# Optimization experiments

Measured on AMD Instinct MI355X. Metric: run time of the kernel, lower is better.

## Reference

```python
import jax, jax.numpy as jnp
import numpy as np


def _div_tree_level(n_agents, level):
    # Deterministic reproduction of get_division_tree (seeded shuffle), row `level`.
    rng = np.random.RandomState(0)
    perm = rng.permutation(n_agents)
    max_div = int(np.ceil(np.log2(n_agents)))
    levels = np.zeros((max_div + 1, n_agents), dtype=np.int64)
    for ith in range(1, max_div + 1):
        levels[ith] = levels[ith - 1]
        for j in range(n_agents):
            seg = j // (n_agents / 2 ** ith)
            if int(seg) % 2 == 1:
                levels[ith, j] += 2 ** (ith - 1)
    res = levels[:, perm]  # res_levels[:, i] = levels[:, agent2divitreeindex[i]]
    return res[level]


def setup_inputs() -> dict:
    B, A, D, H, NA = 4096, 32, 512, 512, 32
    LEVEL = 3  # current_level after change_div_tree_level(3): 8 distinct experts
    key = jax.random.key(0)
    ks = jax.random.split(key, 4)
    x0 = jax.random.normal(ks[0], (B, A, D), dtype=jnp.float32)
    W_shared = jax.random.normal(ks[1], (D, H), dtype=jnp.float32) * 0.02
    b_shared = jnp.zeros((H,), jnp.float32)
    W1 = jax.random.normal(ks[2], (A, H, H), dtype=jnp.float32) * 0.02
    b1 = jnp.zeros((A, H), jnp.float32)
    W2 = jax.random.normal(ks[3], (A, H, NA), dtype=jnp.float32) * 0.02
    b2 = jnp.zeros((A, NA), jnp.float32)
    route = jnp.asarray(_div_tree_level(A, LEVEL), dtype=jnp.int32)  # [A] expert id per agent
    return dict(x0=x0, W_shared=W_shared, b_shared=b_shared,
                W1=W1, b1=b1, W2=W2, b2=b2, route=route)


def reference(x0, W_shared, b_shared, W1, b1, W2, b2, route):
    # shared trunk: Linear + ReLU over all agents at once
    x1 = jax.nn.relu(x0 @ W_shared + b_shared)          # [B, A, H]
    # static MoE dispatch: gather each agent's expert weights, batched GEMM per agent slot
    Wg1, bg1 = W1[route], b1[route]                     # [A, H, H], [A, H]
    Wg2, bg2 = W2[route], b2[route]                     # [A, H, NA], [A, NA]
    h = jax.nn.relu(jnp.einsum('bah,ahk->bak', x1, Wg1) + bg1)   # [B, A, H]
    x2 = jnp.einsum('bah,ahk->bak', h, Wg2) + bg2       # [B, A, NA]
    return x2
```

## Files before the change

### kernel.cpp

```cpp
#include <hip/hip_runtime.h>
#include <cstdint>
#include <cstddef>

typedef __bf16 bf16x8 __attribute__((ext_vector_type(8)));
typedef float f32x4 __attribute__((ext_vector_type(4)));
typedef unsigned short u16;
typedef u16 u16x4 __attribute__((ext_vector_type(4)));
typedef u16 u16x8 __attribute__((ext_vector_type(8)));

__device__ __forceinline__ u16 f2bf(float f) {
  union { float f; unsigned u; } v; v.f = f;
  return (u16)((v.u + 0x7FFFu + ((v.u >> 16) & 1u)) >> 16);
}

__global__ void frag_cvt(const float* __restrict__ in, const int* __restrict__ route,
                         u16* __restrict__ out, int K, int N) {
  const int a = blockIdx.z;
  const int src = route ? route[a] : a;
  const int f = threadIdx.x >> 6, l = threadIdx.x & 63;
  const int r = l & 15, q = l >> 4;
  const int kt = blockIdx.x * 4 + f;
  const int nb = blockIdx.y;
  const int KT = K >> 5, NB = N >> 4;
  const float* ip = in + (size_t)src * K * N + (size_t)(kt * 32 + q * 8) * N + nb * 16 + r;
  u16x8 d;
#pragma unroll
  for (int e = 0; e < 8; ++e) d[e] = f2bf(ip[(size_t)e * N]);
  *(u16x8*)&out[((((size_t)a * NB + nb) * KT + kt) * 64 + l) * 8] = d;
}

__device__ __forceinline__ void gemm64(const u16* __restrict__ Bw, const u16* __restrict__ Xs,
                                       int r, int q, f32x4 acc[4][4]) {
  bf16x8 bcur[4], bnxt[4];
#pragma unroll
  for (int nt = 0; nt < 4; ++nt) bcur[nt] = *(const bf16x8*)(Bw + nt * 8192);
#pragma unroll
  for (int kt = 0; kt < 16; ++kt) {
    if (kt < 15) {
#pragma unroll
      for (int nt = 0; nt < 4; ++nt)
        bnxt[nt] = *(const bf16x8*)(Bw + nt * 8192 + (kt + 1) * 512);
    }
#pragma unroll
    for (int mt = 0; mt < 4; ++mt) {
      const int m = mt * 16 + r;
      const bf16x8 af = *(const bf16x8*)&Xs[m * 512 + ((((kt << 2) + q) ^ (m & 7)) << 3)];
#pragma unroll
      for (int nt = 0; nt < 4; ++nt)
        acc[mt][nt] = __builtin_amdgcn_mfma_f32_16x16x32_bf16(bcur[nt], af, acc[mt][nt], 0, 0, 0);
    }
#pragma unroll
    for (int nt = 0; nt < 4; ++nt) bcur[nt] = bnxt[nt];
  }
}

__device__ __forceinline__ void epi_relu(u16* __restrict__ Xs, const float* __restrict__ bias,
                                         f32x4 acc[4][4], int w, int r, int q) {
#pragma unroll
  for (int mt = 0; mt < 4; ++mt) {
    const int m = mt * 16 + r;
#pragma unroll
    for (int nt = 0; nt < 4; ++nt) {
      const int col = w * 64 + nt * 16 + q * 4;
      const int gp = (col >> 3) ^ (m & 7);
      const float4 bb = *(const float4*)&bias[col];
      const f32x4 v = acc[mt][nt];
      const u16x4 d = { f2bf(fmaxf(v.x + bb.x, 0.f)), f2bf(fmaxf(v.y + bb.y, 0.f)),
                        f2bf(fmaxf(v.z + bb.z, 0.f)), f2bf(fmaxf(v.w + bb.w, 0.f)) };
      *(u16x4*)&Xs[m * 512 + gp * 8 + (q & 1) * 4] = d;
    }
  }
}

__global__ __launch_bounds__(512, 4)
void fused_mlp(const float* __restrict__ X0, const u16* __restrict__ Wsf,
               const float* __restrict__ bsh, const u16* __restrict__ W1f,
               const float* __restrict__ b1, const u16* __restrict__ W2f,
               const float* __restrict__ b2, const int* __restrict__ route,
               float* __restrict__ Out) {
  __shared__ u16 Xs[64 * 512];

  const int tid = threadIdx.x;
  const int w = tid >> 6, l = tid & 63;
  const int r = l & 15, q = l >> 4;

  const int bid = blockIdx.x;
  const int xcd = bid & 7, idx = bid >> 3;
  const int a = (xcd << 2) | (idx >> 6);
  const int b0 = (idx & 63) << 6;
  const int rt = route[a];

  {
    const float* gx = X0 + ((size_t)b0 * 32 + a) * 512;
#pragma unroll
    for (int i = 0; i < 8; ++i) {
      const int lin = i * 512 + tid;
      const int m = lin >> 6, g = lin & 63;
      const float* p = gx + (size_t)m * (32 * 512) + g * 8;
      const float4 u = *(const float4*)p;
      const float4 v = *(const float4*)(p + 4);
      const u16x8 d = { f2bf(u.x), f2bf(u.y), f2bf(u.z), f2bf(u.w),
                        f2bf(v.x), f2bf(v.y), f2bf(v.z), f2bf(v.w) };
      *(u16x8*)&Xs[m * 512 + ((g ^ (m & 7)) << 3)] = d;
    }
  }
  __syncthreads();

  f32x4 acc[4][4];

#pragma unroll
  for (int mt = 0; mt < 4; ++mt)
#pragma unroll
    for (int nt = 0; nt < 4; ++nt) acc[mt][nt] = (f32x4){0.f, 0.f, 0.f, 0.f};
  gemm64(Wsf + (w << 15) + l * 8, Xs, r, q, acc);
  __syncthreads();
  epi_relu(Xs, bsh, acc, w, r, q);
  __syncthreads();

#pragma unroll
  for (int mt = 0; mt < 4; ++mt)
#pragma unroll
    for (int nt = 0; nt < 4; ++nt) acc[mt][nt] = (f32x4){0.f, 0.f, 0.f, 0.f};
  gemm64(W1f + (size_t)a * 262144 + (w << 15) + l * 8, Xs, r, q, acc);
  __syncthreads();
  epi_relu(Xs, b1 + (size_t)rt * 512, acc, w, r, q);
  __syncthreads();

  {
    const int mt3 = w & 3, nt3 = w >> 2;
    const int m = mt3 * 16 + r;
    const u16* B2 = W2f + (size_t)a * 16384 + (nt3 << 13) + l * 8;
    f32x4 o = (f32x4){0.f, 0.f, 0.f, 0.f};
#pragma unroll
    for (int kt = 0; kt < 16; ++kt) {
      const bf16x8 af = *(const bf16x8*)&Xs[m * 512 + ((((kt << 2) + q) ^ (m & 7)) << 3)];
      const bf16x8 bf = *(const bf16x8*)(B2 + (kt << 9));
      o = __builtin_amdgcn_mfma_f32_16x16x32_bf16(bf, af, o, 0, 0, 0);
    }
    const int col = (nt3 << 4) + (q << 2);
    const float4 bb = *(const float4*)&b2[rt * 32 + col];
    const float4 res = { o.x + bb.x, o.y + bb.y, o.z + bb.z, o.w + bb.w };
    *(float4*)&Out[(size_t)(b0 + m) * 1024 + a * 32 + col] = res;
  }
}

extern "C" void kernel_launch(void* const* d_in, const int* in_sizes, int n_in,
                              void* d_out, int out_size, void* d_ws, size_t ws_size,
                              hipStream_t stream) {
  (void)in_sizes; (void)n_in; (void)out_size; (void)ws_size;
  const float* x0  = (const float*)d_in[0];
  const float* Wsh = (const float*)d_in[1];
  const float* bsh = (const float*)d_in[2];
  const float* W1  = (const float*)d_in[3];
  const float* b1  = (const float*)d_in[4];
  const float* W2  = (const float*)d_in[5];
  const float* b2  = (const float*)d_in[6];
  const int* route = (const int*)d_in[7];
  float* out = (float*)d_out;

  char* ws = (char*)d_ws;
  u16* Wsf = (u16*)(ws + 0);
  u16* W1f = (u16*)(ws + 524288);
  u16* W2f = (u16*)(ws + 524288 + 16777216);

  frag_cvt<<<dim3(4, 32, 1),  256, 0, stream>>>(Wsh, nullptr, Wsf, 512, 512);
  frag_cvt<<<dim3(4, 32, 32), 256, 0, stream>>>(W1, route, W1f, 512, 512);
  frag_cvt<<<dim3(4, 2, 32),  256, 0, stream>>>(W2, route, W2f, 512, 32);
  fused_mlp<<<dim3(2048), 512, 0, stream>>>(x0, Wsf, bsh, W1f, b1, W2f, b2, route, out);
}
```

Measured before the change: 555.0 us.

## Double batch tile per block, fragment-major LDS layout, convert only routed experts

The fused MLP kernel now uses 1024-thread blocks covering 128 batch rows per agent, split into 2 M-warpgroups by 8 N-warps. Each weight fragment loaded from global memory is therefore reused across twice as many rows. Activations in LDS are stored in MFMA-fragment-major order instead of a swizzled row layout, so A-fragment loads become contiguous. The weight conversion now converts each distinct expert once, indexed by expert id, and skips experts no agent uses, which cuts redundant conversion traffic. In exchange, the block uses 128KB of LDS and 1024 threads, so occupancy is lower and the grid has fewer blocks.

```diff
diff --git a/kernel.cpp b/kernel.cpp
--- a/kernel.cpp
+++ b/kernel.cpp
@@ -13,24 +13,29 @@
   return (u16)((v.u + 0x7FFFu + ((v.u >> 16) & 1u)) >> 16);
 }
 
-__global__ void frag_cvt(const float* __restrict__ in, const int* __restrict__ route,
+__global__ void frag_cvt(const float* __restrict__ in, const int* __restrict__ sel,
                          u16* __restrict__ out, int K, int N) {
-  const int a = blockIdx.z;
-  const int src = route ? route[a] : a;
+  const int s = blockIdx.z;
+  if (sel) {
+    bool need = false;
+#pragma unroll
+    for (int i = 0; i < 32; ++i) need |= (sel[i] == s);
+    if (!need) return;
+  }
   const int f = threadIdx.x >> 6, l = threadIdx.x & 63;
   const int r = l & 15, q = l >> 4;
   const int kt = blockIdx.x * 4 + f;
   const int nb = blockIdx.y;
   const int KT = K >> 5, NB = N >> 4;
-  const float* ip = in + (size_t)src * K * N + (size_t)(kt * 32 + q * 8) * N + nb * 16 + r;
+  const float* ip = in + (size_t)s * K * N + (size_t)(kt * 32 + q * 8) * N + nb * 16 + r;
   u16x8 d;
 #pragma unroll
   for (int e = 0; e < 8; ++e) d[e] = f2bf(ip[(size_t)e * N]);
-  *(u16x8*)&out[((((size_t)a * NB + nb) * KT + kt) * 64 + l) * 8] = d;
+  *(u16x8*)&out[((((size_t)s * NB + nb) * KT + kt) * 64 + l) * 8] = d;
 }
 
-__device__ __forceinline__ void gemm64(const u16* __restrict__ Bw, const u16* __restrict__ Xs,
-                                       int r, int q, f32x4 acc[4][4]) {
+__device__ __forceinline__ void gemm64(const u16* __restrict__ Bw, const u16* __restrict__ Af,
+                                       f32x4 acc[4][4]) {
   bf16x8 bcur[4], bnxt[4];
 #pragma unroll
   for (int nt = 0; nt < 4; ++nt) bcur[nt] = *(const bf16x8*)(Bw + nt * 8192);
@@ -43,8 +48,7 @@
     }
 #pragma unroll
     for (int mt = 0; mt < 4; ++mt) {
-      const int m = mt * 16 + r;
-      const bf16x8 af = *(const bf16x8*)&Xs[m * 512 + ((((kt << 2) + q) ^ (m & 7)) << 3)];
+      const bf16x8 af = *(const bf16x8*)(Af + kt * 4096 + mt * 512);
 #pragma unroll
       for (int nt = 0; nt < 4; ++nt)
         acc[mt][nt] = __builtin_amdgcn_mfma_f32_16x16x32_bf16(bcur[nt], af, acc[mt][nt], 0, 0, 0);
@@ -55,92 +59,95 @@
 }
 
 __device__ __forceinline__ void epi_relu(u16* __restrict__ Xs, const float* __restrict__ bias,
-                                         f32x4 acc[4][4], int w, int r, int q) {
+                                         f32x4 acc[4][4], int wm, int wn, int r, int q) {
 #pragma unroll
   for (int mt = 0; mt < 4; ++mt) {
-    const int m = mt * 16 + r;
+    const int MT = wm * 4 + mt;
 #pragma unroll
     for (int nt = 0; nt < 4; ++nt) {
-      const int col = w * 64 + nt * 16 + q * 4;
-      const int gp = (col >> 3) ^ (m & 7);
+      const int col = wn * 64 + nt * 16 + q * 4;
+      const int kt2 = col >> 5;
+      const int q2 = (col >> 3) & 3;
       const float4 bb = *(const float4*)&bias[col];
       const f32x4 v = acc[mt][nt];
       const u16x4 d = { f2bf(fmaxf(v.x + bb.x, 0.f)), f2bf(fmaxf(v.y + bb.y, 0.f)),
                         f2bf(fmaxf(v.z + bb.z, 0.f)), f2bf(fmaxf(v.w + bb.w, 0.f)) };
-      *(u16x4*)&Xs[m * 512 + gp * 8 + (q & 1) * 4] = d;
+      *(u16x4*)&Xs[((kt2 * 8 + MT) * 64 + q2 * 16 + r) * 8 + (q & 1) * 4] = d;
     }
   }
 }
 
-__global__ __launch_bounds__(512, 4)
+__global__ __launch_bounds__(1024, 4)
 void fused_mlp(const float* __restrict__ X0, const u16* __restrict__ Wsf,
                const float* __restrict__ bsh, const u16* __restrict__ W1f,
                const float* __restrict__ b1, const u16* __restrict__ W2f,
                const float* __restrict__ b2, const int* __restrict__ route,
                float* __restrict__ Out) {
-  __shared__ u16 Xs[64 * 512];
+  __shared__ u16 Xs[65536];
 
   const int tid = threadIdx.x;
   const int w = tid >> 6, l = tid & 63;
   const int r = l & 15, q = l >> 4;
+  const int wm = w >> 3, wn = w & 7;
 
   const int bid = blockIdx.x;
   const int xcd = bid & 7, idx = bid >> 3;
-  const int a = (xcd << 2) | (idx >> 6);
-  const int b0 = (idx & 63) << 6;
+  const int a = (xcd << 2) | (idx >> 5);
+  const int b0 = (idx & 31) << 7;
   const int rt = route[a];
 
   {
-    const float* gx = X0 + ((size_t)b0 * 32 + a) * 512;
+    const int m = ((w & 7) << 4) + r;
+    const float* p = X0 + ((size_t)b0 * 32 + a) * 512 + (size_t)m * 16384
+                   + ((w >> 3) << 8) + (q << 3);
+    const int ktb = (w >> 3) << 3;
 #pragma unroll
     for (int i = 0; i < 8; ++i) {
-      const int lin = i * 512 + tid;
-      const int m = lin >> 6, g = lin & 63;
-      const float* p = gx + (size_t)m * (32 * 512) + g * 8;
-      const float4 u = *(const float4*)p;
-      const float4 v = *(const float4*)(p + 4);
+      const float4 u = *(const float4*)(p + i * 32);
+      const float4 v = *(const float4*)(p + i * 32 + 4);
       const u16x8 d = { f2bf(u.x), f2bf(u.y), f2bf(u.z), f2bf(u.w),
                         f2bf(v.x), f2bf(v.y), f2bf(v.z), f2bf(v.w) };
-      *(u16x8*)&Xs[m * 512 + ((g ^ (m & 7)) << 3)] = d;
+      *(u16x8*)&Xs[((ktb + i) * 8 + (w & 7)) * 512 + l * 8] = d;
     }
   }
   __syncthreads();
 
   f32x4 acc[4][4];
+  const u16* Af = Xs + (wm << 11) + l * 8;
 
 #pragma unroll
   for (int mt = 0; mt < 4; ++mt)
 #pragma unroll
     for (int nt = 0; nt < 4; ++nt) acc[mt][nt] = (f32x4){0.f, 0.f, 0.f, 0.f};
-  gemm64(Wsf + (w << 15) + l * 8, Xs, r, q, acc);
+  gemm64(Wsf + (wn << 15) + l * 8, Af, acc);
   __syncthreads();
-  epi_relu(Xs, bsh, acc, w, r, q);
+  epi_relu(Xs, bsh, acc, wm, wn, r, q);
   __syncthreads();
 
 #pragma unroll
   for (int mt = 0; mt < 4; ++mt)
 #pragma unroll
     for (int nt = 0; nt < 4; ++nt) acc[mt][nt] = (f32x4){0.f, 0.f, 0.f, 0.f};
-  gemm64(W1f + (size_t)a * 262144 + (w << 15) + l * 8, Xs, r, q, acc);
+  gemm64(W1f + ((size_t)rt << 18) + (wn << 15) + l * 8, Af, acc);
   __syncthreads();
-  epi_relu(Xs, b1 + (size_t)rt * 512, acc, w, r, q);
+  epi_relu(Xs, b1 + (size_t)rt * 512, acc, wm, wn, r, q);
   __syncthreads();
 
   {
-    const int mt3 = w & 3, nt3 = w >> 2;
-    const int m = mt3 * 16 + r;
-    const u16* B2 = W2f + (size_t)a * 16384 + (nt3 << 13) + l * 8;
+    const int mtg = w >> 1, nt3 = w & 1;
+    const u16* Ah = Xs + (mtg << 9) + l * 8;
+    const u16* B2 = W2f + ((size_t)rt << 14) + (nt3 << 13) + l * 8;
     f32x4 o = (f32x4){0.f, 0.f, 0.f, 0.f};
 #pragma unroll
     for (int kt = 0; kt < 16; ++kt) {
-      const bf16x8 af = *(const bf16x8*)&Xs[m * 512 + ((((kt << 2) + q) ^ (m & 7)) << 3)];
-      const bf16x8 bf = *(const bf16x8*)(B2 + (kt << 9));
+      const bf16x8 af = *(const bf16x8*)(Ah + kt * 4096);
+      const bf16x8 bf = *(const bf16x8*)(B2 + kt * 512);
       o = __builtin_amdgcn_mfma_f32_16x16x32_bf16(bf, af, o, 0, 0, 0);
     }
     const int col = (nt3 << 4) + (q << 2);
     const float4 bb = *(const float4*)&b2[rt * 32 + col];
     const float4 res = { o.x + bb.x, o.y + bb.y, o.z + bb.z, o.w + bb.w };
-    *(float4*)&Out[(size_t)(b0 + m) * 1024 + a * 32 + col] = res;
+    *(float4*)&Out[(size_t)(b0 + (mtg << 4) + r) * 1024 + a * 32 + col] = res;
   }
 }
 
@@ -166,5 +173,5 @@
   frag_cvt<<<dim3(4, 32, 1),  256, 0, stream>>>(Wsh, nullptr, Wsf, 512, 512);
   frag_cvt<<<dim3(4, 32, 32), 256, 0, stream>>>(W1, route, W1f, 512, 512);
   frag_cvt<<<dim3(4, 2, 32),  256, 0, stream>>>(W2, route, W2f, 512, 32);
-  fused_mlp<<<dim3(2048), 512, 0, stream>>>(x0, Wsf, bsh, W1f, b1, W2f, b2, route, out);
+  fused_mlp<<<dim3(1024), 1024, 0, stream>>>(x0, Wsf, bsh, W1f, b1, W2f, b2, route, out);
 }
```

Result: slower. 613.5 us (+10.6%).
